# Kernel optimization log

Hardware: AMD Instinct MI355X
Metric: run time of the kernel (lower is better)

The kernel has to match this reference:

```python
import jax, jax.numpy as jnp
import numpy as np

B, S = 64, 512
NQ, RAW, D, H, K = 10000, 256, 256, 64, 4  # vocab, raw emb, model emb, gru state, num_stages
LN_EPS = 1e-5


def setup_inputs() -> dict:
    key = jax.random.key(0)
    ks = jax.random.split(key, 30)
    def n(i, shape, s=0.02):
        return (jax.random.normal(ks[i], shape) * s).astype(jnp.float32)
    return {
        "q": jax.random.randint(ks[0], (B, S), 0, NQ, dtype=jnp.int32),
        "r": jax.random.randint(ks[1], (B, S), 0, 2, dtype=jnp.int32),
        # flattened 4-stage embedding table [NQ*4, RAW]
        "emb_table": n(2, (NQ * K, RAW)),
        # per-stage expert MLPs (weights stored as [in, out])
        "expert_w1": n(3, (K, RAW, RAW)), "expert_b1": n(4, (K, RAW)),
        "expert_w2": n(5, (K, RAW, D)),  "expert_b2": n(6, (K, D)),
        # router input adapter Linear(RAW*4 -> D)
        "adapter_w": n(7, (RAW * K, D)), "adapter_b": n(8, (D,)),
        # interaction reducer Linear(2D -> H)
        "reducer_w": n(9, (2 * D, H)), "reducer_b": n(10, (H,)),
        "start_token": jnp.zeros((1, 1, H), jnp.float32),
        # torch GRU params: [3H, in], gate order (r, z, n)
        "gru_w_ih": n(11, (3 * H, H)), "gru_w_hh": n(12, (3 * H, H)),
        "gru_b_ih": n(13, (3 * H,)),   "gru_b_hh": n(14, (3 * H,)),
        # gate Linear(D+H -> 4)
        "wgate_w": n(15, (D + H, K)), "wgate_b": n(16, (K,)),
        "ln_gamma": jnp.ones((D,), jnp.float32), "ln_beta": jnp.zeros((D,), jnp.float32),
        "resp_table": n(17, (2, D)),
        "proj_cor_w": n(18, (D, D)), "proj_cor_b": n(19, (D,)),
        "proj_inc_w": n(20, (D, D)), "proj_inc_b": n(21, (D,)),
    }


def _forward(q, r, emb_table, expert_w1, expert_b1, expert_w2, expert_b2,
             adapter_w, adapter_b, reducer_w, reducer_b, start_token,
             gru_w_ih, gru_w_hh, gru_b_ih, gru_b_hh, wgate_w, wgate_b,
             ln_gamma, ln_beta, resp_table, proj_cor_w, proj_cor_b,
             proj_inc_w, proj_inc_b):
    b, s = q.shape
    # 4-stage embedding lookup: indices q*4 + [0..3]
    stage_idx = q[..., None] * K + jnp.arange(K)          # [B,S,4]
    q_raw = emb_table[stage_idx]                          # [B,S,4,RAW]
    # smart summary (router input adapter), eval mode -> no dropout
    q_flat = q_raw.reshape(b, s, K * RAW)
    q_summary = jax.nn.relu(q_flat @ adapter_w + adapter_b)  # [B,S,D]
    r_emb = resp_table[r]                                    # [B,S,D]
    gru_in = jnp.concatenate([q_summary, r_emb], -1) @ reducer_w + reducer_b  # [B,S,H]
    start = jnp.broadcast_to(start_token, (b, 1, H))
    x = jnp.concatenate([start, gru_in[:, :-1]], axis=1)     # shifted [B,S,H]
    # GRU over time (torch gate order r,z,n)
    xg = x @ gru_w_ih.T + gru_b_ih                           # [B,S,3H]
    def step(h, xg_t):
        hg = h @ gru_w_hh.T + gru_b_hh
        xr, xz, xn = jnp.split(xg_t, 3, axis=-1)
        hr, hz, hn = jnp.split(hg, 3, axis=-1)
        rg = jax.nn.sigmoid(xr + hr)
        zg = jax.nn.sigmoid(xz + hz)
        ng = jnp.tanh(xn + rg * hn)
        h_new = (1.0 - zg) * ng + zg * h
        return h_new, h_new
    _, m = jax.lax.scan(step, jnp.zeros((b, H), x.dtype), xg.transpose(1, 0, 2))
    m_seq = m.transpose(1, 0, 2)                             # [B,S,H]
    # parallel experts (vectorized over the 4 stages)
    h1 = jax.nn.relu(jnp.einsum('bske,keh->bskh', q_raw, expert_w1) + expert_b1)
    experts = jnp.einsum('bskh,khd->bskd', h1, expert_w2) + expert_b2  # [B,S,4,D]
    # noisy routing (eval: no noise), top-1 mask, softmax gating
    logits = jnp.concatenate([q_summary, m_seq], -1) @ wgate_w + wgate_b  # [B,S,4]
    gate_probs = jax.nn.softmax(logits, axis=-1)
    top1 = jnp.argmax(logits, axis=-1)
    onehot = jax.nn.one_hot(top1, K, dtype=logits.dtype)
    masked = jnp.where(onehot > 0, logits, -jnp.inf)
    gate_w = jax.nn.softmax(masked, axis=-1)                 # one-hot for top_k=1
    combined = jnp.einsum('bskd,bsk->bsd', experts, gate_w)  # [B,S,D]
    # layer norm
    mu = combined.mean(-1, keepdims=True)
    var = combined.var(-1, keepdims=True)
    q_fused = ln_gamma * (combined - mu) * jax.lax.rsqrt(var + LN_EPS) + ln_beta
    emb_cor = q_fused @ proj_cor_w + proj_cor_b
    emb_inc = q_fused @ proj_inc_w + proj_inc_b
    rm = r[..., None].astype(q_fused.dtype)
    qa_fused = emb_cor * rm + emb_inc * (1.0 - rm)
    return q_fused, qa_fused, gate_probs


def reference(q, r, emb_table, expert_w1, expert_b1, expert_w2, expert_b2,
              adapter_w, adapter_b, reducer_w, reducer_b, start_token,
              gru_w_ih, gru_w_hh, gru_b_ih, gru_b_hh, wgate_w, wgate_b,
              ln_gamma, ln_beta, resp_table, proj_cor_w, proj_cor_b,
              proj_inc_w, proj_inc_b):
    q_fused, qa_fused, _ = _forward(q, r, emb_table, expert_w1, expert_b1,
                                    expert_w2, expert_b2, adapter_w, adapter_b,
                                    reducer_w, reducer_b, start_token,
                                    gru_w_ih, gru_w_hh, gru_b_ih, gru_b_hh,
                                    wgate_w, wgate_b, ln_gamma, ln_beta,
                                    resp_table, proj_cor_w, proj_cor_b,
                                    proj_inc_w, proj_inc_b)
    return (q_fused, qa_fused)
```

## Files before the change

### kernel.cpp

```cpp
#include <hip/hip_runtime.h>
#include <cstddef>


#define NQ 10000
#define TT 32768

typedef __attribute__((ext_vector_type(8))) short bf16x8;
typedef __attribute__((ext_vector_type(4))) float f32x4;

__device__ double g_qs  [NQ * 256];
__device__ double g_xgr [2 * 192];
__device__ float  g_xg0f[192];
__device__ float  g_xq2 [NQ * 384];
__device__ double g_lq  [NQ * 4];
__device__ float  g_m   [TT * 64];
__device__ unsigned short g_w1t  [4 * 256 * 256];
__device__ unsigned short g_w2t  [4 * 256 * 256];
__device__ unsigned short g_projt[512 * 256];
__device__ unsigned short g_qf   [NQ * 4 * 256];

__device__ __forceinline__ float bf2f(unsigned short x) {
  return __uint_as_float(((unsigned)x) << 16);
}
__device__ __forceinline__ unsigned short f2bf(float f) {
  unsigned u = __float_as_uint(f);
  u += 0x7FFFu + ((u >> 16) & 1u);
  return (unsigned short)(u >> 16);
}
__device__ __forceinline__ f32x4 mfma16(bf16x8 a, bf16x8 b, f32x4 c) {
  return __builtin_amdgcn_mfma_f32_16x16x32_bf16(a, b, c, 0, 0, 0);
}
__device__ __forceinline__ void pkfma(float2& c, float2 a, float2 b) {
  asm("v_pk_fma_f32 %0, %1, %2, %0" : "+v"(c) : "v"(a), "v"(b));
}

__device__ __forceinline__ double fexp(double x) {
  const double L2E  = 1.4426950408889634074;
  const double LN2H = 6.93147180369123816490e-01;
  const double LN2L = 1.90821492927058770002e-10;
  double n = rint(x * L2E);
  int ni = (int)n;
  double r = fma(-n, LN2H, x);
  r = fma(-n, LN2L, r);
  double p = 2.7557319223985888e-07;
  p = fma(p, r, 2.7557319223985893e-06);
  p = fma(p, r, 2.4801587301587302e-05);
  p = fma(p, r, 1.9841269841269841e-04);
  p = fma(p, r, 1.3888888888888889e-03);
  p = fma(p, r, 8.3333333333333332e-03);
  p = fma(p, r, 4.1666666666666664e-02);
  p = fma(p, r, 1.6666666666666666e-01);
  p = fma(p, r, 0.5);
  p = fma(p, r, 1.0);
  p = fma(p, r, 1.0);
  return ldexp(p, ni);
}

__device__ __forceinline__ double tpoly(double p) {
  const double p2 = p * p;
  double t = -1382.0 / 155925.0;
  t = fma(t, p2, 62.0 / 2835.0);
  t = fma(t, p2, -17.0 / 315.0);
  t = fma(t, p2, 2.0 / 15.0);
  t = fma(t, p2, -1.0 / 3.0);
  t = fma(t, p2, 1.0);
  return p * t;
}

__global__ void __launch_bounds__(256) prepqsk_kernel(
    const float* __restrict__ expert_w1, const float* __restrict__ expert_w2,
    const float* __restrict__ proj_cor_w, const float* __restrict__ proj_inc_w,
    const float* __restrict__ resp_table, const float* __restrict__ reducer_w,
    const float* __restrict__ reducer_b,  const float* __restrict__ start_token,
    const float* __restrict__ gru_w_ih,   const float* __restrict__ gru_b_ih,
    const float* __restrict__ emb, const float* __restrict__ adapter_w,
    const float* __restrict__ adapter_b)
{
  __shared__ double red2f[128];
  __shared__ __align__(16) float As[64][33];
  __shared__ __align__(16) float Bs[32][65];
  const int tid = threadIdx.x;

  if (blockIdx.x < 64) {
    if (blockIdx.x == 0) {
      if (tid < 128) {
        const int rr = tid >> 6, j = tid & 63;
        double acc = (double)reducer_b[j];
        for (int k = 0; k < 256; ++k)
          acc += (double)resp_table[rr * 256 + k] *
                 (double)reducer_w[(256 + k) * 64 + j];
        red2f[tid] = acc;
      }
      __syncthreads();
      if (tid < 192) {
        const double bih = (double)gru_b_ih[tid];
        double a0 = bih, a1 = bih, a2 = bih;
        for (int j = 0; j < 64; ++j) {
          const double w = (double)gru_w_ih[tid * 64 + j];
          a0 += red2f[j] * w;
          a1 += red2f[64 + j] * w;
          a2 += (double)start_token[j] * w;
        }
        g_xgr[tid] = a0; g_xgr[192 + tid] = a1; g_xg0f[tid] = (float)a2;
      }
    }
    const int idx0 = blockIdx.x * 256 + tid;
    const int stride = 64 * 256;
    for (int i = idx0; i < 4 * 256 * 256; i += stride) {
      const int e = i >> 16, rem = i & 65535, n = rem >> 8, k = rem & 255;
      g_w1t[i] = f2bf(expert_w1[e * 65536 + k * 256 + n]);
      g_w2t[i] = f2bf(expert_w2[e * 65536 + k * 256 + n]);
    }
    for (int i = idx0; i < 512 * 256; i += stride) {
      const int n = i >> 8, k = i & 255;
      g_projt[i] = f2bf((n < 256) ? proj_cor_w[k * 256 + n]
                                  : proj_inc_w[k * 256 + (n - 256)]);
    }
    return;
  }

  const int bq = blockIdx.x - 64;
  const int q0 = (bq >> 2) * 64;
  const int n0 = (bq & 3) * 64;
  const int ty = tid >> 4, tx = tid & 15;

  double acc[4][4];
#pragma unroll
  for (int i = 0; i < 4; ++i)
#pragma unroll
    for (int j = 0; j < 4; ++j) acc[i][j] = 0.0;

  const int arow = tid >> 2, aks = (tid & 3) * 8;
  const int qa = min(q0 + arow, NQ - 1);
  const int bkk = tid >> 3, bns = (tid & 7) * 8;

  for (int kc = 0; kc < 1024; kc += 32) {
    f32x4 av0 = *(const f32x4*)(emb + (size_t)qa * 1024 + kc + aks);
    f32x4 av1 = *(const f32x4*)(emb + (size_t)qa * 1024 + kc + aks + 4);
    f32x4 bv0 = *(const f32x4*)(adapter_w + (size_t)(kc + bkk) * 256 + n0 + bns);
    f32x4 bv1 = *(const f32x4*)(adapter_w + (size_t)(kc + bkk) * 256 + n0 + bns + 4);
    __syncthreads();
#pragma unroll
    for (int i = 0; i < 4; ++i) { As[arow][aks + i] = av0[i]; As[arow][aks + 4 + i] = av1[i]; }
#pragma unroll
    for (int i = 0; i < 4; ++i) { Bs[bkk][bns + i] = bv0[i]; Bs[bkk][bns + 4 + i] = bv1[i]; }
    __syncthreads();
#pragma unroll 4
    for (int kk = 0; kk < 32; ++kk) {
      double a[4], b[4];
#pragma unroll
      for (int i = 0; i < 4; ++i) a[i] = (double)As[ty * 4 + i][kk];
#pragma unroll
      for (int j = 0; j < 4; ++j) b[j] = (double)Bs[kk][tx * 4 + j];
#pragma unroll
      for (int i = 0; i < 4; ++i)
#pragma unroll
        for (int j = 0; j < 4; ++j) acc[i][j] = fma(a[i], b[j], acc[i][j]);
    }
  }
#pragma unroll
  for (int i = 0; i < 4; ++i) {
    const int qrow = q0 + ty * 4 + i;
    if (qrow < NQ) {
#pragma unroll
      for (int j = 0; j < 4; ++j) {
        const int n = n0 + tx * 4 + j;
        double v = acc[i][j] + (double)adapter_b[n];
        g_qs[(size_t)qrow * 256 + n] = v > 0.0 ? v : 0.0;
      }
    }
  }
}

__global__ void __launch_bounds__(256) smallk_kernel(
    const float* __restrict__ reducer_w, const float* __restrict__ gru_w_ih,
    const float* __restrict__ wgate_w)
{
  __shared__ double qsr[256];
  __shared__ double ps[4][64];
  __shared__ double gi[64];
  const int tid = threadIdx.x;
  const int qq = blockIdx.x;
  qsr[tid] = g_qs[(size_t)qq * 256 + tid];
  __syncthreads();
  {
    const int j = tid & 63, h = tid >> 6;
    const int k0 = h * 64;
    double a0 = 0.0, a1 = 0.0, a2 = 0.0, a3 = 0.0;
    for (int k = 0; k < 64; k += 4) {
      a0 = fma(qsr[k0 + k + 0], (double)reducer_w[(k0 + k + 0) * 64 + j], a0);
      a1 = fma(qsr[k0 + k + 1], (double)reducer_w[(k0 + k + 1) * 64 + j], a1);
      a2 = fma(qsr[k0 + k + 2], (double)reducer_w[(k0 + k + 2) * 64 + j], a2);
      a3 = fma(qsr[k0 + k + 3], (double)reducer_w[(k0 + k + 3) * 64 + j], a3);
    }
    ps[h][j] = (a0 + a1) + (a2 + a3);
  }
  __syncthreads();
  if (tid < 64) gi[tid] = (ps[0][tid] + ps[1][tid]) + (ps[2][tid] + ps[3][tid]);
  if (tid >= 64 && tid < 68) {
    const int e = tid - 64;
    double a0 = 0.0, a1 = 0.0, a2 = 0.0, a3 = 0.0;
    for (int k = 0; k < 256; k += 4) {
      a0 = fma(qsr[k + 0], (double)wgate_w[(k + 0) * 4 + e], a0);
      a1 = fma(qsr[k + 1], (double)wgate_w[(k + 1) * 4 + e], a1);
      a2 = fma(qsr[k + 2], (double)wgate_w[(k + 2) * 4 + e], a2);
      a3 = fma(qsr[k + 3], (double)wgate_w[(k + 3) * 4 + e], a3);
    }
    g_lq[(size_t)qq * 4 + e] = (a0 + a1) + (a2 + a3);
  }
  __syncthreads();
  if (tid < 192) {
    double a0 = 0.0, a1 = 0.0, a2 = 0.0, a3 = 0.0;
    for (int k = 0; k < 64; k += 4) {
      a0 = fma(gi[k + 0], (double)gru_w_ih[tid * 64 + k + 0], a0);
      a1 = fma(gi[k + 1], (double)gru_w_ih[tid * 64 + k + 1], a1);
      a2 = fma(gi[k + 2], (double)gru_w_ih[tid * 64 + k + 2], a2);
      a3 = fma(gi[k + 3], (double)gru_w_ih[tid * 64 + k + 3], a3);
    }
    const double s = (a0 + a1) + (a2 + a3);
    g_xq2[(size_t)qq * 384 + tid]       = (float)(s + g_xgr[tid]);
    g_xq2[(size_t)qq * 384 + 192 + tid] = (float)(s + g_xgr[192 + tid]);
  }
}

__global__ void __attribute__((amdgpu_waves_per_eu(1, 1)))
__launch_bounds__(128, 1) gruE_kernel(
    const int* __restrict__ q, const int* __restrict__ r,
    const float* __restrict__ whh, const float* __restrict__ bhh,
    const float* __restrict__ emb,
    const float* __restrict__ b1, const float* __restrict__ b2,
    const float* __restrict__ lng, const float* __restrict__ lnb)
{
  __shared__ __align__(16) float HF[2][68];
  __shared__ __align__(16) unsigned short QR[32 * 264];
  __shared__ __align__(16) unsigned short H1[32 * 264];
  __shared__ __align__(16) unsigned short EO[32 * 264];
  const int tid = threadIdx.x;

  if (blockIdx.x < 64) {
    const int b = blockIdx.x;
    const int wv = tid >> 6;
    const int l = tid & 63;
    const int p = l >> 1;
    const int half = l & 1;
    const int j = wv * 32 + p;
    const int k0 = half * 32;

    float2 Wr[16], Wz[16], Wn[16];
#pragma unroll
    for (int i = 0; i < 16; ++i) {
      Wr[i] = *(const float2*)(whh + (size_t)(0 * 64 + j) * 64 + k0 + 2 * i);
      Wz[i] = *(const float2*)(whh + (size_t)(1 * 64 + j) * 64 + k0 + 2 * i);
      Wn[i] = *(const float2*)(whh + (size_t)(2 * 64 + j) * 64 + k0 + 2 * i);
    }
#pragma unroll
    for (int i = 0; i < 16; ++i) {
      asm volatile("" : "+v"(Wr[i]));
      asm volatile("" : "+v"(Wz[i]));
      asm volatile("" : "+v"(Wn[i]));
    }
    const double br = (double)bhh[j];
    const double bz = (double)bhh[64 + j];
    const double bn = (double)bhh[128 + j];

    float cx0 = g_xg0f[j], cx1 = g_xg0f[64 + j], cx2 = g_xg0f[128 + j];
    int qA = q[b * 512], rA = r[b * 512];

    const int jpad = j + ((j >> 5) << 2);
    if (tid < 64) {
      const int tp = tid + ((tid >> 5) << 2);
      HF[0][tp] = 0.f;
    }
    double hd = 0.0;
    asm volatile("s_waitcnt lgkmcnt(0)\n\ts_barrier" ::: "memory");

    for (int t = 0; t < 512; ++t) {
      float nx0 = 0.f, nx1 = 0.f, nx2 = 0.f;
      int qB = qA, rB = rA;
      if (t < 511) {
        const size_t base = (size_t)(qA * 2 + rA) * 192 + j;
        nx0 = g_xq2[base];
        nx1 = g_xq2[base + 64];
        nx2 = g_xq2[base + 128];
        const int tk = min(t + 1, 510);
        qB = q[b * 512 + tk];
        rB = r[b * 512 + tk];
      }

      float2 ar = {0.f, 0.f}, az = {0.f, 0.f}, an = {0.f, 0.f};
      {
        const float4* hp = (const float4*)&HF[t & 1][half * 36];
#pragma unroll
        for (int g = 0; g < 8; ++g) {
          const float4 t4 = hp[g];
          const float2 hA = make_float2(t4.x, t4.y);
          const float2 hB = make_float2(t4.z, t4.w);
          pkfma(ar, Wr[2 * g], hA); pkfma(ar, Wr[2 * g + 1], hB);
          pkfma(az, Wz[2 * g], hA); pkfma(az, Wz[2 * g + 1], hB);
          pkfma(an, Wn[2 * g], hA); pkfma(an, Wn[2 * g + 1], hB);
        }
      }
      const float srh = ar.x + ar.y;
      const float szh = az.x + az.y;
      const float snh = an.x + an.y;
      const float sro = __shfl_xor(srh, 1);
      const float szo = __shfl_xor(szh, 1);
      const float sno = __shfl_xor(snh, 1);
      const double hr = br + ((double)srh + (double)sro);
      const double hz = bz + ((double)szh + (double)szo);
      const double hn = bn + ((double)snh + (double)sno);
      const double pr = (double)cx0 + hr, pz = (double)cx1 + hz;
      const double xn = (double)cx2;
      double rg = fma(0.5, tpoly(0.5 * pr), 0.5);
      double zg = fma(0.5, tpoly(0.5 * pz), 0.5);
      double pre = fma(rg, hn, xn);
      double ng = tpoly(pre);
      const bool bad = (fabs(pr) > 0.5) | (fabs(pz) > 0.5) | (fabs(pre) > 0.25);
      if (bad) {
        rg = 1.0 / (1.0 + fexp(-pr));
        zg = 1.0 / (1.0 + fexp(-pz));
        pre = fma(rg, hn, xn);
        ng = 1.0 - 2.0 / (fexp(pre + pre) + 1.0);
      }
      const double hnew = fma(zg, hd - ng, ng);
      hd = hnew;
      const float hnf = (float)hnew;
      if (half == 0) {
        HF[(t & 1) ^ 1][jpad] = hnf;
        g_m[((size_t)b * 512 + t) * 64 + j] = hnf;
      }
      asm volatile("s_waitcnt lgkmcnt(0)\n\ts_barrier" ::: "memory");

      cx0 = nx0; cx1 = nx1; cx2 = nx2;
      qA = qB; rA = rB;
    }
    return;
  }

  const int bx = blockIdx.x - 64;
  const int e  = bx & 3;
  const int t0 = (bx >> 2) * 32;
  const int w = tid >> 6;
  const int lane = tid & 63;
  const int l15 = lane & 15;
  const int quad = lane >> 4;

  for (int c = 0; c < 16; ++c) {
    const int idx = c * 128 + tid;
    const int row = idx >> 6, col4 = idx & 63;
    const int qv = min(t0 + row, NQ - 1);
    f32x4 v = *(const f32x4*)(emb + (size_t)qv * 1024 + e * 256 + col4 * 4);
    unsigned a = ((unsigned)f2bf(v[1]) << 16) | f2bf(v[0]);
    unsigned bb = ((unsigned)f2bf(v[3]) << 16) | f2bf(v[2]);
    *(uint2*)&QR[row * 264 + col4 * 4] = make_uint2(a, bb);
  }
  __syncthreads();

  const f32x4 z4 = {0.f, 0.f, 0.f, 0.f};
  const int n0 = w * 128;

  f32x4 acc[2][8];
#pragma unroll
  for (int a = 0; a < 2; ++a)
#pragma unroll
    for (int bq = 0; bq < 8; ++bq) acc[a][bq] = z4;
#pragma unroll
  for (int ks = 0; ks < 8; ++ks) {
    const int koff = ks * 32 + quad * 8;
    bf16x8 a0 = *(const bf16x8*)&QR[l15 * 264 + koff];
    bf16x8 a1 = *(const bf16x8*)&QR[(16 + l15) * 264 + koff];
#pragma unroll
    for (int nt = 0; nt < 8; ++nt) {
      bf16x8 bbv = *(const bf16x8*)(g_w1t + (size_t)e * 65536 +
                                    (size_t)(n0 + nt * 16 + l15) * 256 + koff);
      acc[0][nt] = mfma16(a0, bbv, acc[0][nt]);
      acc[1][nt] = mfma16(a1, bbv, acc[1][nt]);
    }
  }
#pragma unroll
  for (int nt = 0; nt < 8; ++nt) {
    const int n = n0 + nt * 16 + l15;
    const float b1v = b1[e * 256 + n];
#pragma unroll
    for (int mt = 0; mt < 2; ++mt)
#pragma unroll
      for (int rg = 0; rg < 4; ++rg) {
        const int m = mt * 16 + quad * 4 + rg;
        H1[m * 264 + n] = f2bf(fmaxf(acc[mt][nt][rg] + b1v, 0.f));
      }
  }
  __syncthreads();

  f32x4 acc2[2][8];
#pragma unroll
  for (int a = 0; a < 2; ++a)
#pragma unroll
    for (int bq = 0; bq < 8; ++bq) acc2[a][bq] = z4;
#pragma unroll
  for (int ks = 0; ks < 8; ++ks) {
    const int koff = ks * 32 + quad * 8;
    bf16x8 a0 = *(const bf16x8*)&H1[l15 * 264 + koff];
    bf16x8 a1 = *(const bf16x8*)&H1[(16 + l15) * 264 + koff];
#pragma unroll
    for (int nt = 0; nt < 8; ++nt) {
      bf16x8 bbv = *(const bf16x8*)(g_w2t + (size_t)e * 65536 +
                                    (size_t)(n0 + nt * 16 + l15) * 256 + koff);
      acc2[0][nt] = mfma16(a0, bbv, acc2[0][nt]);
      acc2[1][nt] = mfma16(a1, bbv, acc2[1][nt]);
    }
  }
#pragma unroll
  for (int nt = 0; nt < 8; ++nt) {
    const int n = n0 + nt * 16 + l15;
    const float b2v = b2[e * 256 + n];
#pragma unroll
    for (int mt = 0; mt < 2; ++mt)
#pragma unroll
      for (int rg = 0; rg < 4; ++rg) {
        const int m = mt * 16 + quad * 4 + rg;
        EO[m * 264 + n] = f2bf(acc2[mt][nt][rg] + b2v);
      }
  }
  __syncthreads();

  {
    const int m = tid >> 2;
    const int sub = tid & 3;
    float sx = 0.f, sxx = 0.f;
#pragma unroll
    for (int i = 0; i < 8; ++i) {
      bf16x8 v = *(const bf16x8*)&EO[m * 264 + sub * 64 + i * 8];
#pragma unroll
      for (int c = 0; c < 8; ++c) {
        const float f = bf2f((unsigned short)v[c]);
        sx += f; sxx += f * f;
      }
    }
    sx += __shfl_xor(sx, 1); sxx += __shfl_xor(sxx, 1);
    sx += __shfl_xor(sx, 2); sxx += __shfl_xor(sxx, 2);
    const float mu = sx * (1.f / 256.f);
    const float var = sxx * (1.f / 256.f) - mu * mu;
    const float inv = 1.f / sqrtf(var + 1e-5f);
    if (t0 + m < NQ) {
      const size_t base = ((size_t)(t0 + m) * 4 + e) * 256;
#pragma unroll
      for (int i = 0; i < 8; ++i) {
        const int dbase = sub * 64 + i * 8;
        bf16x8 v = *(const bf16x8*)&EO[m * 264 + dbase];
        bf16x8 ov;
#pragma unroll
        for (int c = 0; c < 8; ++c) {
          const int d = dbase + c;
          const float f = bf2f((unsigned short)v[c]);
          ov[c] = (short)f2bf(lng[d] * (f - mu) * inv + lnb[d]);
        }
        *(bf16x8*)(g_qf + base + dbase) = ov;
      }
    }
  }
}

__global__ void __launch_bounds__(128) kernelF(
    const int* __restrict__ q, const int* __restrict__ r,
    const float* __restrict__ wgate_w, const float* __restrict__ wgate_b,
    const float* __restrict__ pcb, const float* __restrict__ pib,
    float* __restrict__ out)
{
  __shared__ __align__(16) unsigned short QF[32 * 264];
  __shared__ double w2d[256];
  __shared__ int rv_l[32];
  const int tid = threadIdx.x;
  const int t0 = blockIdx.x * 32;
  const int w = tid >> 6;
  const int lane = tid & 63;
  const int l15 = lane & 15;
  const int quad = lane >> 4;
  if (tid < 32) rv_l[tid] = r[t0 + tid];
  w2d[tid] = (double)wgate_w[1024 + tid];
  w2d[128 + tid] = (double)wgate_w[1152 + tid];
  __syncthreads();

  int bi;
  {
    const int tok = tid >> 2;
    const int e = tid & 3;
    const int t = t0 + tok;
    const int qv = q[t];
    double le = g_lq[(size_t)qv * 4 + e] + (double)wgate_b[e];
    const f32x4* mr4 = (const f32x4*)(g_m + (size_t)t * 64);
#pragma unroll 4
    for (int jj = 0; jj < 16; ++jj) {
      const f32x4 mv4 = mr4[jj];
#pragma unroll
      for (int c = 0; c < 4; ++c)
        le = fma((double)mv4[c], w2d[(jj * 4 + c) * 4 + e], le);
    }
    double v = le; bi = e;
    {
      const double vo = __shfl_xor(v, 1);
      const int bo = __shfl_xor(bi, 1);
      const bool ilow = (e & 1) == 0;
      const double vl = ilow ? v : vo, vh = ilow ? vo : v;
      const int bl = ilow ? bi : bo, bh = ilow ? bo : bi;
      if (vh > vl) { v = vh; bi = bh; } else { v = vl; bi = bl; }
    }
    {
      const double vo = __shfl_xor(v, 2);
      const int bo = __shfl_xor(bi, 2);
      const bool ilow = (e & 2) == 0;
      const double vl = ilow ? v : vo, vh = ilow ? vo : v;
      const int bl = ilow ? bi : bo, bh = ilow ? bo : bi;
      if (vh > vl) { v = vh; bi = bh; } else { v = vl; bi = bl; }
    }
  }

  {
    const int m = tid >> 2;
    const size_t row = ((size_t)q[t0 + m] * 4 + bi) * 256;
#pragma unroll
    for (int i = 0; i < 8; ++i) {
      const int dbase = (tid & 3) * 64 + i * 8;
      bf16x8 v = *(const bf16x8*)(g_qf + row + dbase);
      *(bf16x8*)&QF[m * 264 + dbase] = v;
      f32x4 f0, f1;
#pragma unroll
      for (int c = 0; c < 4; ++c) f0[c] = bf2f((unsigned short)v[c]);
#pragma unroll
      for (int c = 0; c < 4; ++c) f1[c] = bf2f((unsigned short)v[4 + c]);
      *(f32x4*)(out + (size_t)(t0 + m) * 256 + dbase) = f0;
      *(f32x4*)(out + (size_t)(t0 + m) * 256 + dbase + 4) = f1;
    }
  }
  __syncthreads();

  const f32x4 z4 = {0.f, 0.f, 0.f, 0.f};
  const int n0 = w * 128;
  for (int ph = 0; ph < 2; ++ph) {
    f32x4 acc[2][8];
#pragma unroll
    for (int a = 0; a < 2; ++a)
#pragma unroll
      for (int bq = 0; bq < 8; ++bq) acc[a][bq] = z4;
#pragma unroll
    for (int ks = 0; ks < 8; ++ks) {
      const int koff = ks * 32 + quad * 8;
      bf16x8 a0 = *(const bf16x8*)&QF[l15 * 264 + koff];
      bf16x8 a1 = *(const bf16x8*)&QF[(16 + l15) * 264 + koff];
#pragma unroll
      for (int nt = 0; nt < 8; ++nt) {
        bf16x8 bbv = *(const bf16x8*)(g_projt +
            (size_t)(ph * 256 + n0 + nt * 16 + l15) * 256 + koff);
        acc[0][nt] = mfma16(a0, bbv, acc[0][nt]);
        acc[1][nt] = mfma16(a1, bbv, acc[1][nt]);
      }
    }
    const float* pbb = ph ? pib : pcb;
    const int want = ph ? 0 : 1;
#pragma unroll
    for (int nt = 0; nt < 8; ++nt) {
      const int n = n0 + nt * 16 + l15;
      const float pbv = pbb[n];
#pragma unroll
      for (int mt = 0; mt < 2; ++mt)
#pragma unroll
        for (int rg = 0; rg < 4; ++rg) {
          const int m = mt * 16 + quad * 4 + rg;
          if (rv_l[m] == want)
            out[(size_t)TT * 256 + (size_t)(t0 + m) * 256 + n] =
                acc[mt][nt][rg] + pbv;
        }
    }
  }
}

extern "C" void kernel_launch(void* const* d_in, const int* in_sizes, int n_in,
                              void* d_out, int out_size, void* d_ws, size_t ws_size,
                              hipStream_t stream)
{
  const int*   q   = (const int*)d_in[0];
  const int*   r   = (const int*)d_in[1];
  const float* emb = (const float*)d_in[2];
  const float* ew1 = (const float*)d_in[3];
  const float* eb1 = (const float*)d_in[4];
  const float* ew2 = (const float*)d_in[5];
  const float* eb2 = (const float*)d_in[6];
  const float* aw  = (const float*)d_in[7];
  const float* ab  = (const float*)d_in[8];
  const float* rw  = (const float*)d_in[9];
  const float* rb  = (const float*)d_in[10];
  const float* st  = (const float*)d_in[11];
  const float* wih = (const float*)d_in[12];
  const float* whh = (const float*)d_in[13];
  const float* bih = (const float*)d_in[14];
  const float* bhh = (const float*)d_in[15];
  const float* wgw = (const float*)d_in[16];
  const float* wgb = (const float*)d_in[17];
  const float* lng = (const float*)d_in[18];
  const float* lnb = (const float*)d_in[19];
  const float* resp= (const float*)d_in[20];
  const float* pcw = (const float*)d_in[21];
  const float* pcb = (const float*)d_in[22];
  const float* piw = (const float*)d_in[23];
  const float* pib = (const float*)d_in[24];
  float* out = (float*)d_out;
  (void)bih; (void)in_sizes; (void)n_in; (void)d_ws; (void)ws_size; (void)out_size;

  prepqsk_kernel<<<692, 256, 0, stream>>>(ew1, ew2, pcw, piw, resp, rw, rb, st,
                                          wih, bih, emb, aw, ab);
  smallk_kernel<<<NQ, 256, 0, stream>>>(rw, wih, wgw);
  gruE_kernel<<<64 + 313 * 4, 128, 0, stream>>>(q, r, whh, bhh,
                                                emb, eb1, eb2, lng, lnb);
  kernelF<<<1024, 128, 0, stream>>>(q, r, wgw, wgb, pcb, pib, out);
}
```

Measured before the change: 764.7 us.

## Run GRU recurrence in a single wavefront without barriers or cross-lane shuffles

The recurrent GRU blocks now use one 64-lane wave, with each lane computing the full 64-wide hidden dot products for its output unit. This replaces the two-wave split-K scheme, which needed lane-pair shuffles and a workgroup barrier on every timestep, and it drops LDS double-buffering. Input-gate prefetch is also moved two timesteps ahead. In exchange each lane holds twice as many weight registers and runs a dependent FMA chain twice as long per step. Correctness relies on one wave's lanes reading the shared hidden state in lockstep order.

Result: slower. 802.2 us (+4.9%).

```diff
diff --git a/kernel.cpp b/kernel.cpp
--- a/kernel.cpp
+++ b/kernel.cpp
@@ -231,30 +231,26 @@
     const float* __restrict__ b1, const float* __restrict__ b2,
     const float* __restrict__ lng, const float* __restrict__ lnb)
 {
-  __shared__ __align__(16) float HF[2][68];
+  __shared__ __align__(16) float HF[64];
   __shared__ __align__(16) unsigned short QR[32 * 264];
   __shared__ __align__(16) unsigned short H1[32 * 264];
   __shared__ __align__(16) unsigned short EO[32 * 264];
   const int tid = threadIdx.x;
 
   if (blockIdx.x < 64) {
+    if (tid >= 64) return;
+    const int j = tid;
     const int b = blockIdx.x;
-    const int wv = tid >> 6;
-    const int l = tid & 63;
-    const int p = l >> 1;
-    const int half = l & 1;
-    const int j = wv * 32 + p;
-    const int k0 = half * 32;
-
-    float2 Wr[16], Wz[16], Wn[16];
-#pragma unroll
-    for (int i = 0; i < 16; ++i) {
-      Wr[i] = *(const float2*)(whh + (size_t)(0 * 64 + j) * 64 + k0 + 2 * i);
-      Wz[i] = *(const float2*)(whh + (size_t)(1 * 64 + j) * 64 + k0 + 2 * i);
-      Wn[i] = *(const float2*)(whh + (size_t)(2 * 64 + j) * 64 + k0 + 2 * i);
-    }
-#pragma unroll
-    for (int i = 0; i < 16; ++i) {
+
+    float2 Wr[32], Wz[32], Wn[32];
+#pragma unroll
+    for (int i = 0; i < 32; ++i) {
+      Wr[i] = *(const float2*)(whh + (size_t)(0 * 64 + j) * 64 + 2 * i);
+      Wz[i] = *(const float2*)(whh + (size_t)(1 * 64 + j) * 64 + 2 * i);
+      Wn[i] = *(const float2*)(whh + (size_t)(2 * 64 + j) * 64 + 2 * i);
+    }
+#pragma unroll
+    for (int i = 0; i < 32; ++i) {
       asm volatile("" : "+v"(Wr[i]));
       asm volatile("" : "+v"(Wz[i]));
       asm volatile("" : "+v"(Wn[i]));
@@ -264,34 +260,32 @@
     const double bn = (double)bhh[128 + j];
 
     float cx0 = g_xg0f[j], cx1 = g_xg0f[64 + j], cx2 = g_xg0f[128 + j];
-    int qA = q[b * 512], rA = r[b * 512];
-
-    const int jpad = j + ((j >> 5) << 2);
-    if (tid < 64) {
-      const int tp = tid + ((tid >> 5) << 2);
-      HF[0][tp] = 0.f;
-    }
+    int q1 = q[b * 512], r1 = r[b * 512];
+    float nx0, nx1, nx2;
+    {
+      const size_t base = (size_t)(q1 * 2 + r1) * 192 + j;
+      nx0 = g_xq2[base]; nx1 = g_xq2[base + 64]; nx2 = g_xq2[base + 128];
+    }
+    int q2 = q[b * 512 + 1], r2 = r[b * 512 + 1];
+
+    HF[j] = 0.f;
     double hd = 0.0;
-    asm volatile("s_waitcnt lgkmcnt(0)\n\ts_barrier" ::: "memory");
 
     for (int t = 0; t < 512; ++t) {
-      float nx0 = 0.f, nx1 = 0.f, nx2 = 0.f;
-      int qB = qA, rB = rA;
-      if (t < 511) {
-        const size_t base = (size_t)(qA * 2 + rA) * 192 + j;
-        nx0 = g_xq2[base];
-        nx1 = g_xq2[base + 64];
-        nx2 = g_xq2[base + 128];
-        const int tk = min(t + 1, 510);
-        qB = q[b * 512 + tk];
-        rB = r[b * 512 + tk];
+      float mx0 = 0.f, mx1 = 0.f, mx2 = 0.f;
+      int qn = q2, rn = r2;
+      if (t < 510) {
+        const size_t base = (size_t)(q2 * 2 + r2) * 192 + j;
+        mx0 = g_xq2[base]; mx1 = g_xq2[base + 64]; mx2 = g_xq2[base + 128];
+        const int tk = min(t + 2, 510);
+        qn = q[b * 512 + tk]; rn = r[b * 512 + tk];
       }
 
       float2 ar = {0.f, 0.f}, az = {0.f, 0.f}, an = {0.f, 0.f};
       {
-        const float4* hp = (const float4*)&HF[t & 1][half * 36];
-#pragma unroll
-        for (int g = 0; g < 8; ++g) {
+        const float4* hp = (const float4*)HF;
+#pragma unroll
+        for (int g = 0; g < 16; ++g) {
           const float4 t4 = hp[g];
           const float2 hA = make_float2(t4.x, t4.y);
           const float2 hB = make_float2(t4.z, t4.w);
@@ -300,15 +294,9 @@
           pkfma(an, Wn[2 * g], hA); pkfma(an, Wn[2 * g + 1], hB);
         }
       }
-      const float srh = ar.x + ar.y;
-      const float szh = az.x + az.y;
-      const float snh = an.x + an.y;
-      const float sro = __shfl_xor(srh, 1);
-      const float szo = __shfl_xor(szh, 1);
-      const float sno = __shfl_xor(snh, 1);
-      const double hr = br + ((double)srh + (double)sro);
-      const double hz = bz + ((double)szh + (double)szo);
-      const double hn = bn + ((double)snh + (double)sno);
+      const double hr = br + (double)(ar.x + ar.y);
+      const double hz = bz + (double)(az.x + az.y);
+      const double hn = bn + (double)(an.x + an.y);
       const double pr = (double)cx0 + hr, pz = (double)cx1 + hz;
       const double xn = (double)cx2;
       double rg = fma(0.5, tpoly(0.5 * pr), 0.5);
@@ -325,14 +313,12 @@
       const double hnew = fma(zg, hd - ng, ng);
       hd = hnew;
       const float hnf = (float)hnew;
-      if (half == 0) {
-        HF[(t & 1) ^ 1][jpad] = hnf;
-        g_m[((size_t)b * 512 + t) * 64 + j] = hnf;
-      }
-      asm volatile("s_waitcnt lgkmcnt(0)\n\ts_barrier" ::: "memory");
+      HF[j] = hnf;
+      g_m[((size_t)b * 512 + t) * 64 + j] = hnf;
 
       cx0 = nx0; cx1 = nx1; cx2 = nx2;
-      qA = qB; rA = rB;
+      nx0 = mx0; nx1 = mx1; nx2 = mx2;
+      q2 = qn; r2 = rn;
     }
     return;
   }
```
